# Performance work log

Measured on AMD Instinct MI355X. Metric: run time of the kernel, lower is better.

Reference implementation:

```python
import jax, jax.numpy as jnp
import numpy as np

B, T, C, H = 2, 2048, 1024, 16
D = C // H  # head_dim = 64

def setup_inputs() -> dict:
    key = jax.random.key(0)
    k1, k2, k3 = jax.random.split(key, 3)
    x = jax.random.normal(k1, (B, T, C), dtype=jnp.float32)
    W_attn = jax.random.normal(k2, (C, 3 * C), dtype=jnp.float32) * (1.0 / np.sqrt(C))
    W_proj = jax.random.normal(k3, (C, C), dtype=jnp.float32) * (1.0 / np.sqrt(C))
    return {"x": x, "W_attn": W_attn, "W_proj": W_proj}

def reference(x, W_attn, W_proj):
    b, t, c = x.shape
    qkv = x @ W_attn                       # [B,T,3C]
    q, k, v = jnp.split(qkv, 3, axis=-1)
    # [B,T,C] -> [B,H,T,D]
    q = q.reshape(b, t, H, D).transpose(0, 2, 1, 3)
    k = k.reshape(b, t, H, D).transpose(0, 2, 1, 3)
    v = v.reshape(b, t, H, D).transpose(0, 2, 1, 3)
    scale = 1.0 / np.sqrt(D).astype(np.float32)
    att = jnp.einsum('bhqd,bhkd->bhqk', q, k) * scale   # [B,H,T,T]
    causal = jnp.tril(jnp.ones((t, t), dtype=bool))
    att = jnp.where(causal[None, None], att, -jnp.inf)
    att = jax.nn.softmax(att, axis=-1)
    y = jnp.einsum('bhqk,bhkd->bhqd', att, v)           # [B,H,T,D]
    y = y.transpose(0, 2, 1, 3).reshape(b, t, c)        # [B,T,C]
    return y @ W_proj
```

## Files before the change

### kernel.cpp

```cpp
#include <hip/hip_runtime.h>
#include <hip/hip_bf16.h>
#include <cstdint>
#include <cstddef>
#include <cmath>

typedef __attribute__((ext_vector_type(8))) short short8v;
typedef __attribute__((ext_vector_type(4))) float f32x4;
typedef __attribute__((ext_vector_type(4))) unsigned short ushort4v;

__device__ __forceinline__ unsigned short f2bf(float f) {
  union { float f; uint32_t u; } v; v.f = f;
  uint32_t u = v.u;
  return (unsigned short)((u + 0x7fffu + ((u >> 16) & 1u)) >> 16);
}

__device__ __forceinline__ float bf2f(unsigned short u) {
  union { uint32_t u; float f; } v; v.u = ((uint32_t)u) << 16; return v.f;
}

__device__ __forceinline__ uint32_t pack2bf(float a, float b) {
  __hip_bfloat162 h = __float22bfloat162_rn(make_float2(a, b));
  union { __hip_bfloat162 h; uint32_t u; } c; c.h = h; return c.u;
}

__device__ __forceinline__ void load_lds_16B(const void* g, void* l) {
  __builtin_amdgcn_global_load_lds((const __attribute__((address_space(1))) void*)g,
                                   (__attribute__((address_space(3))) void*)l, 16, 0, 0);
}

__global__ __launch_bounds__(256) void cvt_bf16_kernel(const float* __restrict__ src,
                                                       unsigned short* __restrict__ dst,
                                                       int n8) {
  int i = blockIdx.x * 256 + threadIdx.x;
  if (i >= n8) return;
  const float4* s4 = (const float4*)src + (size_t)i * 2;
  float4 f0 = s4[0], f1 = s4[1];
  short8v o;
  o[0] = (short)f2bf(f0.x); o[1] = (short)f2bf(f0.y);
  o[2] = (short)f2bf(f0.z); o[3] = (short)f2bf(f0.w);
  o[4] = (short)f2bf(f1.x); o[5] = (short)f2bf(f1.y);
  o[6] = (short)f2bf(f1.z); o[7] = (short)f2bf(f1.w);
  *(short8v*)(dst + (size_t)i * 8) = o;
}

__global__ __launch_bounds__(256) void transpose_bf16_kernel(const float* __restrict__ W,
                                                             unsigned short* __restrict__ WT,
                                                             int K, int N) {
  __shared__ float tile[64][65];
  int n0 = blockIdx.x * 64, k0 = blockIdx.y * 64;
  int tid = threadIdx.x;
#pragma unroll
  for (int i = 0; i < 4; ++i) {
    int idx = i * 256 + tid;
    int r = idx >> 4, c4 = (idx & 15) * 4;
    float4 v = *(const float4*)(W + (size_t)(k0 + r) * N + n0 + c4);
    tile[r][c4] = v.x; tile[r][c4 + 1] = v.y; tile[r][c4 + 2] = v.z; tile[r][c4 + 3] = v.w;
  }
  __syncthreads();
#pragma unroll
  for (int i = 0; i < 4; ++i) {
    int idx = i * 256 + tid;
    int nr = idx >> 4, k4 = (idx & 15) * 4;
    ushort4 o;
    o.x = f2bf(tile[k4 + 0][nr]);
    o.y = f2bf(tile[k4 + 1][nr]);
    o.z = f2bf(tile[k4 + 2][nr]);
    o.w = f2bf(tile[k4 + 3][nr]);
    *(ushort4*)(WT + (size_t)(n0 + nr) * K + k0 + k4) = o;
  }
}

__global__ __launch_bounds__(256) void transpose_v_kernel(const unsigned short* __restrict__ qkv,
                                                          unsigned short* __restrict__ VT) {
  int bid = blockIdx.x;
  int b = bid >> 9, h = (bid >> 5) & 15, tc = bid & 31;
  __shared__ unsigned short tile[64][68];
  int tid = threadIdx.x;
  const unsigned short* src = qkv + (size_t)(b * 2048 + tc * 64) * 3072 + 2048 + h * 64;
#pragma unroll
  for (int p = 0; p < 4; ++p) {
    int idx = p * 256 + tid;
    int r = idx >> 4, c4 = (idx & 15) * 4;
    *(ushort4*)&tile[r][c4] = *(const ushort4*)(src + (size_t)r * 3072 + c4);
  }
  __syncthreads();
  unsigned short* dst = VT + (size_t)(b * 16 + h) * 64 * 2048 + tc * 64;
#pragma unroll
  for (int p = 0; p < 4; ++p) {
    int idx = p * 256 + tid;
    int d = idx >> 4, k = idx & 15;
    int t4 = k * 4;
    int c4 = ((k >> 3) << 5) | ((k & 3) << 3) | (k & 4);
    ushort4 o;
    o.x = tile[t4][d]; o.y = tile[t4 + 1][d]; o.z = tile[t4 + 2][d]; o.w = tile[t4 + 3][d];
    *(ushort4*)(dst + (size_t)d * 2048 + c4) = o;
  }
}

template <int BF16OUT>
__global__ __launch_bounds__(256) void gemm_bt_kernel(const unsigned short* __restrict__ A,
                                                      const unsigned short* __restrict__ BT,
                                                      void* __restrict__ Cout,
                                                      int M, int N, int K) {
  __shared__ __align__(16) char lds[32768];
  char* As = lds;
  char* Bs = lds + 16384;

  int nbn = N >> 7;
  int nwg = gridDim.x;
  int wg = blockIdx.x;
  int per = nwg >> 3;
  int swz = (wg & 7) * per + (wg >> 3);
  int tm = swz / nbn, tn = swz % nbn;

  int tid = threadIdx.x;
  int wid = tid >> 6, lane = tid & 63;
  int l15 = lane & 15, lhi = lane >> 4;
  int wm = wid >> 1, wn = wid & 1;

  const unsigned short* Abase = A + (size_t)(tm * 128) * K;
  const unsigned short* Bbase = BT + (size_t)(tn * 128) * K;

  size_t ofs[4];
#pragma unroll
  for (int i = 0; i < 4; ++i) {
    int row = i * 32 + (tid >> 3);
    int ss = (tid & 7) ^ (row & 7);
    ofs[i] = (size_t)row * K + ss * 8;
  }

  f32x4 acc[4][4] = {};

  for (int kt = 0; kt < K; kt += 64) {
    __syncthreads();
#pragma unroll
    for (int i = 0; i < 4; ++i)
      load_lds_16B(Abase + ofs[i] + kt, As + i * 4096 + tid * 16);
#pragma unroll
    for (int i = 0; i < 4; ++i)
      load_lds_16B(Bbase + ofs[i] + kt, Bs + i * 4096 + tid * 16);
    __syncthreads();

#pragma unroll
    for (int ks = 0; ks < 2; ++ks) {
      short8v af[4], bfr[4];
#pragma unroll
      for (int mi = 0; mi < 4; ++mi) {
        int row = wm * 64 + mi * 16 + l15;
        int ss = (ks * 4 + lhi) ^ (row & 7);
        af[mi] = *(const short8v*)(As + row * 128 + ss * 16);
      }
#pragma unroll
      for (int ni = 0; ni < 4; ++ni) {
        int row = wn * 64 + ni * 16 + l15;
        int ss = (ks * 4 + lhi) ^ (row & 7);
        bfr[ni] = *(const short8v*)(Bs + row * 128 + ss * 16);
      }
#pragma unroll
      for (int mi = 0; mi < 4; ++mi)
#pragma unroll
        for (int ni = 0; ni < 4; ++ni)
          acc[mi][ni] = __builtin_amdgcn_mfma_f32_16x16x32_bf16(af[mi], bfr[ni], acc[mi][ni], 0, 0, 0);
    }
  }

#pragma unroll
  for (int mi = 0; mi < 4; ++mi)
#pragma unroll
    for (int ni = 0; ni < 4; ++ni)
#pragma unroll
      for (int r = 0; r < 4; ++r) {
        int row = tm * 128 + wm * 64 + mi * 16 + lhi * 4 + r;
        int col = tn * 128 + wn * 64 + ni * 16 + l15;
        float v = acc[mi][ni][r];
        if (BF16OUT)
          ((unsigned short*)Cout)[(size_t)row * N + col] = f2bf(v);
        else
          ((float*)Cout)[(size_t)row * N + col] = v;
      }
}

__global__ __launch_bounds__(256) void gemm_bt64_kernel(const unsigned short* __restrict__ A,
                                                        const unsigned short* __restrict__ BT,
                                                        float* __restrict__ Cout,
                                                        int M, int N, int K) {
  __shared__ __align__(16) char lds[24576];
  char* As = lds;
  char* Bs = lds + 8192;

  int nbn = N >> 7;
  int nwg = gridDim.x;
  int wg = blockIdx.x;
  int per = nwg >> 3;
  int swz = (wg & 7) * per + (wg >> 3);
  int tm = swz / nbn, tn = swz % nbn;

  int tid = threadIdx.x;
  int wid = tid >> 6, lane = tid & 63;
  int l15 = lane & 15, lhi = lane >> 4;

  const unsigned short* Abase = A + (size_t)(tm * 64) * K;
  const unsigned short* Bbase = BT + (size_t)(tn * 128) * K;

  size_t ofsA[2], ofsB[4];
#pragma unroll
  for (int i = 0; i < 2; ++i) {
    int row = i * 32 + (tid >> 3);
    int ss = (tid & 7) ^ (row & 7);
    ofsA[i] = (size_t)row * K + ss * 8;
  }
#pragma unroll
  for (int i = 0; i < 4; ++i) {
    int row = i * 32 + (tid >> 3);
    int ss = (tid & 7) ^ (row & 7);
    ofsB[i] = (size_t)row * K + ss * 8;
  }

  f32x4 acc[4][2] = {};

  for (int kt = 0; kt < K; kt += 64) {
    __syncthreads();
#pragma unroll
    for (int i = 0; i < 2; ++i)
      load_lds_16B(Abase + ofsA[i] + kt, As + i * 4096 + tid * 16);
#pragma unroll
    for (int i = 0; i < 4; ++i)
      load_lds_16B(Bbase + ofsB[i] + kt, Bs + i * 4096 + tid * 16);
    __syncthreads();

#pragma unroll
    for (int ks = 0; ks < 2; ++ks) {
      short8v af[4], bfr[2];
#pragma unroll
      for (int mi = 0; mi < 4; ++mi) {
        int row = mi * 16 + l15;
        int ss = (ks * 4 + lhi) ^ (row & 7);
        af[mi] = *(const short8v*)(As + row * 128 + ss * 16);
      }
#pragma unroll
      for (int ni = 0; ni < 2; ++ni) {
        int row = wid * 32 + ni * 16 + l15;
        int ss = (ks * 4 + lhi) ^ (row & 7);
        bfr[ni] = *(const short8v*)(Bs + row * 128 + ss * 16);
      }
#pragma unroll
      for (int mi = 0; mi < 4; ++mi)
#pragma unroll
        for (int ni = 0; ni < 2; ++ni)
          acc[mi][ni] = __builtin_amdgcn_mfma_f32_16x16x32_bf16(af[mi], bfr[ni], acc[mi][ni], 0, 0, 0);
    }
  }

#pragma unroll
  for (int mi = 0; mi < 4; ++mi)
#pragma unroll
    for (int ni = 0; ni < 2; ++ni)
#pragma unroll
      for (int r = 0; r < 4; ++r) {
        int row = tm * 64 + mi * 16 + lhi * 4 + r;
        int col = tn * 128 + wid * 32 + ni * 16 + l15;
        Cout[(size_t)row * N + col] = acc[mi][ni][r];
      }
}


__device__ __forceinline__ short8v scale_q(short8v q) {
  short8v r;
#pragma unroll
  for (int j = 0; j < 8; ++j)
    r[j] = (short)f2bf(bf2f((unsigned short)q[j]) * 0.18033688f);
  return r;
}

__device__ __forceinline__ void mask_diag(f32x4 s[4], int q_abs, int k0, int lhi) {
#pragma unroll
  for (int ni = 0; ni < 4; ++ni)
#pragma unroll
    for (int r = 0; r < 4; ++r) {
      int kv = k0 + ni * 16 + lhi * 4 + r;
      if (kv > q_abs) s[ni][r] = -1e30f;
    }
}

__device__ __forceinline__ void exp_p(f32x4 s[4]) {
#pragma unroll
  for (int ni = 0; ni < 4; ++ni)
#pragma unroll
    for (int r = 0; r < 4; ++r)
      s[ni][r] = exp2f(s[ni][r]);
}

__device__ __forceinline__ void repack_pa(const f32x4 s[4], short8v pa[2]) {
#pragma unroll
  for (int ks = 0; ks < 2; ++ks) {
    union { uint32_t u[4]; short8v v; } pk;
    pk.u[0] = pack2bf(s[2 * ks][0], s[2 * ks][1]);
    pk.u[1] = pack2bf(s[2 * ks][2], s[2 * ks][3]);
    pk.u[2] = pack2bf(s[2 * ks + 1][0], s[2 * ks + 1][1]);
    pk.u[3] = pack2bf(s[2 * ks + 1][2], s[2 * ks + 1][3]);
    pa[ks] = pk.v;
  }
}

__global__ __launch_bounds__(256) void attn_kernel(const unsigned short* __restrict__ qkv,
                                                   const unsigned short* __restrict__ VT,
                                                   unsigned short* __restrict__ yb) {
  const int T = 2048, LD = 3072;
  int bid = blockIdx.x;
  int qt = 31 - (bid >> 5);
  int bh = bid & 31;
  int b = bh >> 4, h = bh & 15;

  int tid = threadIdx.x;
  int wid = tid >> 6, lane = tid & 63;
  int l15 = lane & 15, lhi = lane >> 4;

  __shared__ __align__(16) char Ks[2][8192];
  __shared__ __align__(16) char Vt[2][8192];

  union { uint32_t u[4]; short8v v; } ob;
  ob.u[0] = ob.u[1] = ob.u[2] = ob.u[3] = 0x3F803F80u;
  const short8v onesv = ob.v;

  int qrow = qt * 64 + wid * 16 + l15;
  const unsigned short* qp = qkv + (size_t)(b * T + qrow) * LD + h * 64;
  short8v qf[2];
  qf[0] = scale_q(*(const short8v*)(qp + lhi * 8));
  qf[1] = scale_q(*(const short8v*)(qp + 32 + lhi * 8));

  const unsigned short* kbase = qkv + (size_t)b * T * LD + 1024 + h * 64;
  const unsigned short* vtbase = VT + (size_t)(b * 16 + h) * 64 * 2048;

  f32x4 o[4] = {};
  f32x4 lf = {};
  int q_abs = qrow;
  int nt = qt + 1;

  auto stageK = [&](int s) {
#pragma unroll
    for (int i2 = 0; i2 < 2; ++i2) {
      int row = i2 * 32 + (tid >> 3);
      int ss = (tid & 7) ^ (row & 7);
      load_lds_16B(kbase + (size_t)(s * 64 + row) * LD + ss * 8, Ks[s & 1] + i2 * 4096 + tid * 16);
    }
  };
  auto stageV = [&](int s) {
#pragma unroll
    for (int i2 = 0; i2 < 2; ++i2) {
      int row = i2 * 32 + (tid >> 3);
      int ss = (tid & 7) ^ (row & 7);
      load_lds_16B(vtbase + (size_t)row * 2048 + s * 64 + ss * 8, Vt[s & 1] + i2 * 4096 + tid * 16);
    }
  };

  stageK(0); stageV(0);
  __syncthreads();

  for (int s = 0; s < nt; ++s) {
    if (s + 1 < nt) { stageK(s + 1); stageV(s + 1); }

    const char* KC = Ks[s & 1];
    const char* VC = Vt[s & 1];
    int k0 = s * 64;

    f32x4 sv[4] = {};
    __builtin_amdgcn_s_setprio(1);
#pragma unroll
    for (int ks = 0; ks < 2; ++ks)
#pragma unroll
      for (int ni = 0; ni < 4; ++ni) {
        int row = ni * 16 + l15;
        int sl = (ks * 4 + lhi) ^ (row & 7);
        short8v kf = *(const short8v*)(KC + row * 128 + sl * 16);
        sv[ni] = __builtin_amdgcn_mfma_f32_16x16x32_bf16(kf, qf[ks], sv[ni], 0, 0, 0);
      }
    __builtin_amdgcn_s_setprio(0);

    if (s == qt) mask_diag(sv, q_abs, k0, lhi);
    exp_p(sv);

    short8v pa[2];
    repack_pa(sv, pa);

    __builtin_amdgcn_s_setprio(1);
#pragma unroll
    for (int ks = 0; ks < 2; ++ks) {
#pragma unroll
      for (int nd = 0; nd < 4; ++nd) {
        int d = nd * 16 + l15;
        int slv = (ks * 4 + lhi) ^ (d & 7);
        short8v bv = *(const short8v*)(VC + d * 128 + slv * 16);
        o[nd] = __builtin_amdgcn_mfma_f32_16x16x32_bf16(pa[ks], bv, o[nd], 0, 0, 0);
      }
      lf = __builtin_amdgcn_mfma_f32_16x16x32_bf16(pa[ks], onesv, lf, 0, 0, 0);
    }
    __builtin_amdgcn_s_setprio(0);

    __syncthreads();
  }

#pragma unroll
  for (int r = 0; r < 4; ++r) {
    float inv = 1.0f / lf[r];
    int q = qt * 64 + wid * 16 + lhi * 4 + r;
#pragma unroll
    for (int nd = 0; nd < 4; ++nd)
      yb[(size_t)(b * T + q) * 1024 + h * 64 + nd * 16 + l15] = f2bf(o[nd][r] * inv);
  }
}

extern "C" void kernel_launch(void* const* d_in, const int* in_sizes, int n_in,
                              void* d_out, int out_size, void* d_ws, size_t ws_size,
                              hipStream_t stream) {
  const float* x = (const float*)d_in[0];
  const float* Wa = (const float*)d_in[1];
  const float* Wp = (const float*)d_in[2];
  float* out = (float*)d_out;

  char* ws = (char*)d_ws;
  unsigned short* xb  = (unsigned short*)(ws);
  unsigned short* VT  = (unsigned short*)(ws);
  unsigned short* WaT = (unsigned short*)(ws + (size_t)(8u  << 20));
  unsigned short* WpT = (unsigned short*)(ws + (size_t)(14u << 20));
  unsigned short* qkv = (unsigned short*)(ws + (size_t)(16u << 20));
  unsigned short* yb  = (unsigned short*)(ws + (size_t)(40u << 20));

  cvt_bf16_kernel<<<2048, 256, 0, stream>>>(x, xb, 524288);
  transpose_bf16_kernel<<<dim3(48, 16), 256, 0, stream>>>(Wa, WaT, 1024, 3072);
  transpose_bf16_kernel<<<dim3(16, 16), 256, 0, stream>>>(Wp, WpT, 1024, 1024);
  gemm_bt_kernel<1><<<dim3(768), 256, 0, stream>>>(xb, WaT, qkv, 4096, 3072, 1024);
  transpose_v_kernel<<<dim3(1024), 256, 0, stream>>>(qkv, VT);
  attn_kernel<<<dim3(1024), 256, 0, stream>>>(qkv, VT, yb);
  gemm_bt64_kernel<<<dim3(512), 256, 0, stream>>>(yb, WpT, out, 4096, 1024, 1024);
}
```

Before: 109.4 us.

## Merge prep kernels and fuse V transpose into QKV GEMM epilogue

Folds the x conversion and both weight transposes into one prep launch, which removes two kernel launches. The QKV GEMM epilogue now writes Q/K into a narrower 2048-wide buffer and writes V directly in the transposed, swizzled VT layout, so the separate V-transpose kernel and its extra read and write of V are gone. The cost is scattered ushort4 stores for the V part of the epilogue and a more complex output path; attention now reads Q and K with a 2048 stride.

Result: faster. 99.94 us (-8.6%).

```diff
diff --git a/kernel.cpp b/kernel.cpp
--- a/kernel.cpp
+++ b/kernel.cpp
@@ -28,27 +28,35 @@
                                    (__attribute__((address_space(3))) void*)l, 16, 0, 0);
 }
 
-__global__ __launch_bounds__(256) void cvt_bf16_kernel(const float* __restrict__ src,
-                                                       unsigned short* __restrict__ dst,
-                                                       int n8) {
-  int i = blockIdx.x * 256 + threadIdx.x;
-  if (i >= n8) return;
-  const float4* s4 = (const float4*)src + (size_t)i * 2;
-  float4 f0 = s4[0], f1 = s4[1];
-  short8v o;
-  o[0] = (short)f2bf(f0.x); o[1] = (short)f2bf(f0.y);
-  o[2] = (short)f2bf(f0.z); o[3] = (short)f2bf(f0.w);
-  o[4] = (short)f2bf(f1.x); o[5] = (short)f2bf(f1.y);
-  o[6] = (short)f2bf(f1.z); o[7] = (short)f2bf(f1.w);
-  *(short8v*)(dst + (size_t)i * 8) = o;
-}
-
-__global__ __launch_bounds__(256) void transpose_bf16_kernel(const float* __restrict__ W,
-                                                             unsigned short* __restrict__ WT,
-                                                             int K, int N) {
+__global__ __launch_bounds__(256) void prep_kernel(const float* __restrict__ x,
+                                                   unsigned short* __restrict__ xb,
+                                                   const float* __restrict__ Wa,
+                                                   unsigned short* __restrict__ WaT,
+                                                   const float* __restrict__ Wp,
+                                                   unsigned short* __restrict__ WpT) {
   __shared__ float tile[64][65];
-  int n0 = blockIdx.x * 64, k0 = blockIdx.y * 64;
+  int bid = blockIdx.x;
   int tid = threadIdx.x;
+
+  if (bid < 2048) {
+    int i = bid * 256 + tid;
+    const float4* s4 = (const float4*)x + (size_t)i * 2;
+    float4 f0 = s4[0], f1 = s4[1];
+    short8v o;
+    o[0] = (short)f2bf(f0.x); o[1] = (short)f2bf(f0.y);
+    o[2] = (short)f2bf(f0.z); o[3] = (short)f2bf(f0.w);
+    o[4] = (short)f2bf(f1.x); o[5] = (short)f2bf(f1.y);
+    o[6] = (short)f2bf(f1.z); o[7] = (short)f2bf(f1.w);
+    *(short8v*)(xb + (size_t)i * 8) = o;
+    return;
+  }
+
+  int t = bid - 2048;
+  const float* W; unsigned short* WT; int N, n0, k0;
+  if (t < 768) { W = Wa; WT = WaT; N = 3072; n0 = (t % 48) * 64; k0 = (t / 48) * 64; }
+  else { t -= 768; W = Wp; WT = WpT; N = 1024; n0 = (t % 16) * 64; k0 = (t / 16) * 64; }
+  const int K = 1024;
+
 #pragma unroll
   for (int i = 0; i < 4; ++i) {
     int idx = i * 256 + tid;
@@ -70,38 +78,11 @@
   }
 }
 
-__global__ __launch_bounds__(256) void transpose_v_kernel(const unsigned short* __restrict__ qkv,
-                                                          unsigned short* __restrict__ VT) {
-  int bid = blockIdx.x;
-  int b = bid >> 9, h = (bid >> 5) & 15, tc = bid & 31;
-  __shared__ unsigned short tile[64][68];
-  int tid = threadIdx.x;
-  const unsigned short* src = qkv + (size_t)(b * 2048 + tc * 64) * 3072 + 2048 + h * 64;
-#pragma unroll
-  for (int p = 0; p < 4; ++p) {
-    int idx = p * 256 + tid;
-    int r = idx >> 4, c4 = (idx & 15) * 4;
-    *(ushort4*)&tile[r][c4] = *(const ushort4*)(src + (size_t)r * 3072 + c4);
-  }
-  __syncthreads();
-  unsigned short* dst = VT + (size_t)(b * 16 + h) * 64 * 2048 + tc * 64;
-#pragma unroll
-  for (int p = 0; p < 4; ++p) {
-    int idx = p * 256 + tid;
-    int d = idx >> 4, k = idx & 15;
-    int t4 = k * 4;
-    int c4 = ((k >> 3) << 5) | ((k & 3) << 3) | (k & 4);
-    ushort4 o;
-    o.x = tile[t4][d]; o.y = tile[t4 + 1][d]; o.z = tile[t4 + 2][d]; o.w = tile[t4 + 3][d];
-    *(ushort4*)(dst + (size_t)d * 2048 + c4) = o;
-  }
-}
-
-template <int BF16OUT>
-__global__ __launch_bounds__(256) void gemm_bt_kernel(const unsigned short* __restrict__ A,
-                                                      const unsigned short* __restrict__ BT,
-                                                      void* __restrict__ Cout,
-                                                      int M, int N, int K) {
+__global__ __launch_bounds__(256) void gemm_qkv_kernel(const unsigned short* __restrict__ A,
+                                                       const unsigned short* __restrict__ BT,
+                                                       unsigned short* __restrict__ qk,
+                                                       unsigned short* __restrict__ VT) {
+  const int K = 1024, N = 3072;
   __shared__ __align__(16) char lds[32768];
   char* As = lds;
   char* Bs = lds + 16384;
@@ -167,17 +148,24 @@
 #pragma unroll
   for (int mi = 0; mi < 4; ++mi)
 #pragma unroll
-    for (int ni = 0; ni < 4; ++ni)
-#pragma unroll
-      for (int r = 0; r < 4; ++r) {
-        int row = tm * 128 + wm * 64 + mi * 16 + lhi * 4 + r;
-        int col = tn * 128 + wn * 64 + ni * 16 + l15;
-        float v = acc[mi][ni][r];
-        if (BF16OUT)
-          ((unsigned short*)Cout)[(size_t)row * N + col] = f2bf(v);
-        else
-          ((float*)Cout)[(size_t)row * N + col] = v;
-      }
+    for (int ni = 0; ni < 4; ++ni) {
+      int col = tn * 128 + wn * 64 + ni * 16 + l15;
+      int row0 = tm * 128 + wm * 64 + mi * 16 + lhi * 4;
+      if (col < 2048) {
+#pragma unroll
+        for (int r = 0; r < 4; ++r)
+          qk[(size_t)(row0 + r) * 2048 + col] = f2bf(acc[mi][ni][r]);
+      } else {
+        int hl = col - 2048, hh = hl >> 6, d = hl & 63;
+        int bb = row0 >> 11, tl = row0 & 2047;
+        int tc = tl >> 6, k = (tl & 63) >> 2;
+        int c4 = ((k >> 3) << 5) | ((k & 3) << 3) | (k & 4);
+        ushort4 w;
+        w.x = f2bf(acc[mi][ni][0]); w.y = f2bf(acc[mi][ni][1]);
+        w.z = f2bf(acc[mi][ni][2]); w.w = f2bf(acc[mi][ni][3]);
+        *(ushort4*)(VT + ((size_t)((bb * 16 + hh) * 64 + d)) * 2048 + tc * 64 + c4) = w;
+      }
+    }
 }
 
 __global__ __launch_bounds__(256) void gemm_bt64_kernel(const unsigned short* __restrict__ A,
@@ -263,7 +251,6 @@
       }
 }
 
-
 __device__ __forceinline__ short8v scale_q(short8v q) {
   short8v r;
 #pragma unroll
@@ -302,10 +289,10 @@
   }
 }
 
-__global__ __launch_bounds__(256) void attn_kernel(const unsigned short* __restrict__ qkv,
+__global__ __launch_bounds__(256) void attn_kernel(const unsigned short* __restrict__ qk,
                                                    const unsigned short* __restrict__ VT,
                                                    unsigned short* __restrict__ yb) {
-  const int T = 2048, LD = 3072;
+  const int T = 2048, LD = 2048;
   int bid = blockIdx.x;
   int qt = 31 - (bid >> 5);
   int bh = bid & 31;
@@ -323,12 +310,12 @@
   const short8v onesv = ob.v;
 
   int qrow = qt * 64 + wid * 16 + l15;
-  const unsigned short* qp = qkv + (size_t)(b * T + qrow) * LD + h * 64;
+  const unsigned short* qp = qk + (size_t)(b * T + qrow) * LD + h * 64;
   short8v qf[2];
   qf[0] = scale_q(*(const short8v*)(qp + lhi * 8));
   qf[1] = scale_q(*(const short8v*)(qp + 32 + lhi * 8));
 
-  const unsigned short* kbase = qkv + (size_t)b * T * LD + 1024 + h * 64;
+  const unsigned short* kbase = qk + (size_t)b * T * LD + 1024 + h * 64;
   const unsigned short* vtbase = VT + (size_t)(b * 16 + h) * 64 * 2048;
 
   f32x4 o[4] = {};
@@ -419,17 +406,14 @@
 
   char* ws = (char*)d_ws;
   unsigned short* xb  = (unsigned short*)(ws);
-  unsigned short* VT  = (unsigned short*)(ws);
   unsigned short* WaT = (unsigned short*)(ws + (size_t)(8u  << 20));
   unsigned short* WpT = (unsigned short*)(ws + (size_t)(14u << 20));
-  unsigned short* qkv = (unsigned short*)(ws + (size_t)(16u << 20));
+  unsigned short* qk  = (unsigned short*)(ws + (size_t)(16u << 20));
+  unsigned short* VT  = (unsigned short*)(ws + (size_t)(32u << 20));
   unsigned short* yb  = (unsigned short*)(ws + (size_t)(40u << 20));
 
-  cvt_bf16_kernel<<<2048, 256, 0, stream>>>(x, xb, 524288);
-  transpose_bf16_kernel<<<dim3(48, 16), 256, 0, stream>>>(Wa, WaT, 1024, 3072);
-  transpose_bf16_kernel<<<dim3(16, 16), 256, 0, stream>>>(Wp, WpT, 1024, 1024);
-  gemm_bt_kernel<1><<<dim3(768), 256, 0, stream>>>(xb, WaT, qkv, 4096, 3072, 1024);
-  transpose_v_kernel<<<dim3(1024), 256, 0, stream>>>(qkv, VT);
-  attn_kernel<<<dim3(1024), 256, 0, stream>>>(qkv, VT, yb);
+  prep_kernel<<<dim3(3072), 256, 0, stream>>>(x, xb, Wa, WaT, Wp, WpT);
+  gemm_qkv_kernel<<<dim3(768), 256, 0, stream>>>(xb, WaT, qk, VT);
+  attn_kernel<<<dim3(1024), 256, 0, stream>>>(qk, VT, yb);
   gemm_bt64_kernel<<<dim3(512), 256, 0, stream>>>(yb, WpT, out, 4096, 1024, 1024);
 }
```
